# Optimization experiments

Hardware: AMD Instinct MI355X
Metric: run time of the kernel (lower is better)

## Reference

```python
import jax, jax.numpy as jnp
import numpy as np

B, T, E, H, D, V, L = 128, 100, 2048, 1024, 256, 2048, 2


def setup_inputs() -> dict:
    key = jax.random.key(0)
    ks = iter(jax.random.split(key, 32))
    def w(shape, s=0.02):
        return jax.random.normal(next(ks), shape, dtype=jnp.float32) * s
    return {
        "input_seq": jax.random.normal(next(ks), (B, T, E), dtype=jnp.float32),
        "h0": jax.random.normal(next(ks), (B, H), dtype=jnp.float32) * 0.1,
        "dt0": jax.random.normal(next(ks), (B, D), dtype=jnp.float32) * 0.1,
        "w2h_W0": w((E, 4 * H)), "w2h_b0": jnp.zeros((4 * H,), jnp.float32),
        "w2h_W1": w((E + H, 4 * H)), "w2h_b1": jnp.zeros((4 * H,), jnp.float32),
        "w2hr_W0": w((E, D)), "w2hr_b0": jnp.zeros((D,), jnp.float32),
        "w2hr_W1": w((E + H, D)), "w2hr_b1": jnp.zeros((D,), jnp.float32),
        "h2h_W0": w((H, 4 * H)), "h2h_b0": jnp.zeros((4 * H,), jnp.float32),
        "h2h_W1": w((H, 4 * H)), "h2h_b1": jnp.zeros((4 * H,), jnp.float32),
        "h2hr_W0": w((H, D)), "h2hr_b0": jnp.zeros((D,), jnp.float32),
        "h2hr_W1": w((H, D)), "h2hr_b1": jnp.zeros((D,), jnp.float32),
        "dc_W0": w((D, H)), "dc_W1": w((D, H)),
        "out_W": w((L * H, V)), "out_b": jnp.zeros((V,), jnp.float32),
    }


def reference(input_seq, h0, dt0,
              w2h_W0, w2h_b0, w2h_W1, w2h_b1,
              w2hr_W0, w2hr_b0, w2hr_W1, w2hr_b1,
              h2h_W0, h2h_b0, h2h_W1, h2h_b1,
              h2hr_W0, h2hr_b0, h2hr_W1, h2hr_b1,
              dc_W0, dc_W1, out_W, out_b):
    # SC-LSTM decoder (sclstm, n_layer=2, dropout=0, teacher forcing / gen=False)
    w2h = [(w2h_W0, w2h_b0), (w2h_W1, w2h_b1)]
    w2hr = [(w2hr_W0, w2hr_b0), (w2hr_W1, w2hr_b1)]
    h2h = [(h2h_W0, h2h_b0), (h2h_W1, h2h_b1)]
    h2hr = [(h2hr_W0, h2hr_b0), (h2hr_W1, h2hr_b1)]
    dc = [dc_W0, dc_W1]
    alpha = 1.0 / L

    # time-step inputs: SOS one-hot at t=0, then input_seq[:, t-1, :]
    sos = jnp.zeros((B, E), input_seq.dtype).at[:, 0].set(1.0)
    xs = jnp.concatenate([sos[:, None, :], input_seq[:, :-1, :]], axis=1)
    xs = jnp.swapaxes(xs, 0, 1)  # (T, B, E)

    h_init = jnp.stack([h0] * L)   # (L, B, H) -- both h and c init from last_hidden_t0
    c_init = jnp.stack([h0] * L)
    d_init = jnp.stack([dt0] * L)  # (L, B, D)

    def step(carry, x_t):
        h, c, d = carry
        # shared semantic-gate contribution: alpha * sum_i h2h_r[i](h_prev[i])
        r_common = alpha * sum(h[i] @ h2hr[i][0] + h2hr[i][1] for i in range(L))
        new_h, new_c, new_d = [], [], []
        for i in range(L):
            inp = x_t if i == 0 else jnp.concatenate([x_t] + new_h, axis=1)
            g = (inp @ w2h[i][0] + w2h[i][1]) + (h[i] @ h2h[i][0] + h2h[i][1])
            gi, gf, go, gc = jnp.split(g, 4, axis=1)
            gate_i = jax.nn.sigmoid(gi)
            gate_f = jax.nn.sigmoid(gf)
            gate_o = jax.nn.sigmoid(go)
            gate_r = jax.nn.sigmoid(inp @ w2hr[i][0] + w2hr[i][1] + r_common)
            dt = gate_r * d[i]
            cell = gate_f * c[i] + gate_i * jnp.tanh(gc) + jnp.tanh(dt @ dc[i])
            hid = gate_o * jnp.tanh(cell)
            new_h.append(hid); new_c.append(cell); new_d.append(dt)
        out_t = jnp.concatenate(new_h, axis=1) @ out_W + out_b  # (B, V)
        return (jnp.stack(new_h), jnp.stack(new_c), jnp.stack(new_d)), out_t

    _, outs = jax.lax.scan(step, (h_init, c_init, d_init), xs)
    return jnp.swapaxes(outs, 0, 1)  # (B, T, V)
```

## Files before the change

kernel.cpp:

```cpp
#include <hip/hip_runtime.h>

using u16 = unsigned short;
using u32 = unsigned int;
using f32x4 = __attribute__((ext_vector_type(4))) float;
using short8 = __attribute__((ext_vector_type(8))) short;

#define TT 100
#define BB 128
#define EE 2048
#define HH 1024
#define DD 256
#define VV 2048
#define H4 4096
#define NPRE 8704
#define MPRE (TT * BB)

__device__ __forceinline__ float bf2f(u16 u) { return __uint_as_float(((u32)u) << 16); }
__device__ __forceinline__ u16 f2bf(float f) {
  u32 x = __float_as_uint(f);
  x += 0x7fffu + ((x >> 16) & 1u);
  return (u16)(x >> 16);
}
__device__ __forceinline__ float sigm(float x) { return 1.0f / (1.0f + expf(-x)); }

__global__ __launch_bounds__(256) void build_xs(const float* __restrict__ inseq,
                                                u16* __restrict__ xs) {
  const int row = blockIdx.x;
  const int e0 = threadIdx.x << 3;
  const int t = row >> 7, b = row & 127;
  u16 v[8];
  if (t == 0) {
#pragma unroll
    for (int i = 0; i < 8; ++i) v[i] = 0;
    if (e0 == 0) v[0] = 0x3F80;
  } else {
    const float* src = inseq + ((size_t)b * TT + (t - 1)) * EE + e0;
#pragma unroll
    for (int i = 0; i < 8; ++i) v[i] = f2bf(src[i]);
  }
  uint4 o;
  o.x = (u32)v[0] | ((u32)v[1] << 16);
  o.y = (u32)v[2] | ((u32)v[3] << 16);
  o.z = (u32)v[4] | ((u32)v[5] << 16);
  o.w = (u32)v[6] | ((u32)v[7] << 16);
  *(uint4*)(xs + (size_t)row * EE + e0) = o;
}

__global__ __launch_bounds__(256) void tconv(const float* __restrict__ in, int ldin,
                                             u16* __restrict__ out, int ldout) {
  __shared__ float tile[32][33];
  const int k0 = blockIdx.y << 5, n0 = blockIdx.x << 5;
  const int tx = threadIdx.x, ty = threadIdx.y;
#pragma unroll
  for (int i = 0; i < 32; i += 8)
    tile[ty + i][tx] = in[(size_t)(k0 + ty + i) * ldin + n0 + tx];
  __syncthreads();
#pragma unroll
  for (int i = 0; i < 32; i += 8)
    out[(size_t)(n0 + ty + i) * ldout + k0 + tx] = f2bf(tile[tx][ty + i]);
}

__global__ __launch_bounds__(256) void k_biascat(
    const float* w2h_b0, const float* h2h_b0, const float* w2h_b1, const float* h2h_b1,
    const float* w2hr_b0, const float* w2hr_b1, float* biascat) {
  int g = blockIdx.x * 256 + threadIdx.x;
  if (g >= NPRE) return;
  float v;
  if (g < 4096) v = w2h_b0[g] + h2h_b0[g];
  else if (g < 8192) v = w2h_b1[g - 4096] + h2h_b1[g - 4096];
  else if (g < 8448) v = w2hr_b0[g - 8192];
  else v = w2hr_b1[g - 8448];
  biascat[g] = v;
}

__global__ __launch_bounds__(256) void k_init(const float* __restrict__ h0,
                                              const float* __restrict__ dt0,
                                              u16* __restrict__ hist, float* c0, float* c1,
                                              float* d0, float* d1) {
  int g = blockIdx.x * 256 + threadIdx.x;
  int b = g >> 11, j = g & 2047;
  float hv = h0[b * HH + (j & 1023)];
  hist[g] = f2bf(hv);
  if (j < HH) { c0[b * HH + j] = hv; c1[b * HH + j] = hv; }
  if (j < DD) { float dv = dt0[b * DD + j]; d0[b * DD + j] = dv; d1[b * DD + j] = dv; }
}

template <int MODE>
__global__ __launch_bounds__(256) void gemm_big(const u16* __restrict__ A,
                                                const u16* __restrict__ Bt,
                                                const float* __restrict__ bias,
                                                void* __restrict__ Cv, int N, int K) {
  __shared__ __align__(16) u16 lA[128 * 72];
  __shared__ __align__(16) u16 lB[128 * 72];
  const int tid = threadIdx.x;
  const int lane = tid & 63;
  const int wid = tid >> 6;
  const int wr = wid >> 1, wc = wid & 1;
  const int nt = N >> 7;
  const int bm = (blockIdx.x / nt) << 7;
  const int bn = (blockIdx.x % nt) << 7;
  f32x4 acc[4][4] = {};
  const int r = tid >> 1;
  const int kh = (tid & 1) << 5;
  const u16* ga = A + (size_t)(bm + r) * K + kh;
  const u16* gb = Bt + (size_t)(bn + r) * K + kh;
  for (int k0 = 0; k0 < K; k0 += 64) {
    uint4 a0 = *(const uint4*)(ga + k0);
    uint4 a1 = *(const uint4*)(ga + k0 + 8);
    uint4 a2 = *(const uint4*)(ga + k0 + 16);
    uint4 a3 = *(const uint4*)(ga + k0 + 24);
    uint4 b0 = *(const uint4*)(gb + k0);
    uint4 b1 = *(const uint4*)(gb + k0 + 8);
    uint4 b2 = *(const uint4*)(gb + k0 + 16);
    uint4 b3 = *(const uint4*)(gb + k0 + 24);
    __syncthreads();
    *(uint4*)(lA + r * 72 + kh) = a0;
    *(uint4*)(lA + r * 72 + kh + 8) = a1;
    *(uint4*)(lA + r * 72 + kh + 16) = a2;
    *(uint4*)(lA + r * 72 + kh + 24) = a3;
    *(uint4*)(lB + r * 72 + kh) = b0;
    *(uint4*)(lB + r * 72 + kh + 8) = b1;
    *(uint4*)(lB + r * 72 + kh + 16) = b2;
    *(uint4*)(lB + r * 72 + kh + 24) = b3;
    __syncthreads();
#pragma unroll
    for (int ks = 0; ks < 2; ++ks) {
      const int kk = ks * 32 + ((lane >> 4) << 3);
      short8 af[4], bf[4];
#pragma unroll
      for (int i = 0; i < 4; ++i) {
        af[i] = *(const short8*)(lA + (wr * 64 + i * 16 + (lane & 15)) * 72 + kk);
        bf[i] = *(const short8*)(lB + (wc * 64 + i * 16 + (lane & 15)) * 72 + kk);
      }
#pragma unroll
      for (int i = 0; i < 4; ++i)
#pragma unroll
        for (int j = 0; j < 4; ++j)
          acc[i][j] = __builtin_amdgcn_mfma_f32_16x16x32_bf16(af[i], bf[j], acc[i][j], 0, 0, 0);
    }
  }
#pragma unroll
  for (int i = 0; i < 4; ++i) {
#pragma unroll
    for (int j = 0; j < 4; ++j) {
      const int col = bn + wc * 64 + j * 16 + (lane & 15);
      const int rb = bm + wr * 64 + i * 16 + ((lane >> 4) << 2);
      const float bv = bias[col];
#pragma unroll
      for (int rg = 0; rg < 4; ++rg) {
        const int row = rb + rg;
        const float v = acc[i][j][rg] + bv;
        if (MODE == 0) {
          ((u16*)Cv)[(size_t)row * N + col] = f2bf(v);
        } else {
          const int tt = row >> 7, b = row & 127;
          ((float*)Cv)[((size_t)b * TT + tt) * VV + col] = v;
        }
      }
    }
  }
}

__device__ __forceinline__ void gemm64(const u16* __restrict__ A, int lda,
                                       const u16* __restrict__ Bt, int ldb, int K,
                                       u16* lA, u16* lB, f32x4 acc[2][2]) {
  const int tid = threadIdx.x;
  const int lane = tid & 63;
  const int wid = tid >> 6;
  const int wr = wid >> 1, wc = wid & 1;
  const int r = tid >> 2;
  const int kq = (tid & 3) << 4;
  const u16* ga = A + (size_t)r * lda + kq;
  const u16* gb = Bt + (size_t)r * ldb + kq;
  for (int k0 = 0; k0 < K; k0 += 64) {
    uint4 a0 = *(const uint4*)(ga + k0);
    uint4 a1 = *(const uint4*)(ga + k0 + 8);
    uint4 b0 = *(const uint4*)(gb + k0);
    uint4 b1 = *(const uint4*)(gb + k0 + 8);
    __syncthreads();
    *(uint4*)(lA + r * 72 + kq) = a0;
    *(uint4*)(lA + r * 72 + kq + 8) = a1;
    *(uint4*)(lB + r * 72 + kq) = b0;
    *(uint4*)(lB + r * 72 + kq + 8) = b1;
    __syncthreads();
#pragma unroll
    for (int ks = 0; ks < 2; ++ks) {
      const int kk = ks * 32 + ((lane >> 4) << 3);
      const short8 af0 = *(const short8*)(lA + (wr * 32 + (lane & 15)) * 72 + kk);
      const short8 af1 = *(const short8*)(lA + (wr * 32 + 16 + (lane & 15)) * 72 + kk);
      const short8 bf0 = *(const short8*)(lB + (wc * 32 + (lane & 15)) * 72 + kk);
      const short8 bf1 = *(const short8*)(lB + (wc * 32 + 16 + (lane & 15)) * 72 + kk);
      acc[0][0] = __builtin_amdgcn_mfma_f32_16x16x32_bf16(af0, bf0, acc[0][0], 0, 0, 0);
      acc[0][1] = __builtin_amdgcn_mfma_f32_16x16x32_bf16(af0, bf1, acc[0][1], 0, 0, 0);
      acc[1][0] = __builtin_amdgcn_mfma_f32_16x16x32_bf16(af1, bf0, acc[1][0], 0, 0, 0);
      acc[1][1] = __builtin_amdgcn_mfma_f32_16x16x32_bf16(af1, bf1, acc[1][1], 0, 0, 0);
    }
  }
  __syncthreads();
}

__device__ __forceinline__ void gemm_ccA(const u16* __restrict__ Bt, const u16* lA, u16* lB,
                                         f32x4 acc[2][2]) {
  const int tid = threadIdx.x;
  const int lane = tid & 63;
  const int wid = tid >> 6;
  const int wr = wid >> 1, wc = wid & 1;
  const int r = tid >> 2;
  const int kq = (tid & 3) << 4;
  const u16* gb = Bt + (size_t)r * DD + kq;
  for (int k0 = 0; k0 < 256; k0 += 64) {
    uint4 b0 = *(const uint4*)(gb + k0);
    uint4 b1 = *(const uint4*)(gb + k0 + 8);
    __syncthreads();
    *(uint4*)(lB + r * 72 + kq) = b0;
    *(uint4*)(lB + r * 72 + kq + 8) = b1;
    __syncthreads();
#pragma unroll
    for (int ks = 0; ks < 2; ++ks) {
      const int kk = ks * 32 + ((lane >> 4) << 3);
      const int ka = k0 + kk;
      const short8 af0 = *(const short8*)(lA + (wr * 32 + (lane & 15)) * 264 + ka);
      const short8 af1 = *(const short8*)(lA + (wr * 32 + 16 + (lane & 15)) * 264 + ka);
      const short8 bf0 = *(const short8*)(lB + (wc * 32 + (lane & 15)) * 72 + kk);
      const short8 bf1 = *(const short8*)(lB + (wc * 32 + 16 + (lane & 15)) * 72 + kk);
      acc[0][0] = __builtin_amdgcn_mfma_f32_16x16x32_bf16(af0, bf0, acc[0][0], 0, 0, 0);
      acc[0][1] = __builtin_amdgcn_mfma_f32_16x16x32_bf16(af0, bf1, acc[0][1], 0, 0, 0);
      acc[1][0] = __builtin_amdgcn_mfma_f32_16x16x32_bf16(af1, bf0, acc[1][0], 0, 0, 0);
      acc[1][1] = __builtin_amdgcn_mfma_f32_16x16x32_bf16(af1, bf1, acc[1][1], 0, 0, 0);
    }
  }
  __syncthreads();
}

#define EPI(...)                                                          \
  do {                                                                    \
    _Pragma("unroll") for (int ei = 0; ei < 2; ++ei) {                    \
      _Pragma("unroll") for (int ej = 0; ej < 2; ++ej) {                  \
        const int col = n0 + wc * 32 + ej * 16 + (lane & 15);             \
        const int rb = m0 + wr * 32 + ei * 16 + ((lane >> 4) << 2);       \
        _Pragma("unroll") for (int rg = 0; rg < 4; ++rg) {                \
          const int row = rb + rg;                                        \
          const float av = acc[ei][ej][rg];                               \
          __VA_ARGS__                                                     \
        }                                                                 \
      }                                                                   \
    }                                                                     \
  } while (0)

struct SeqArgs {
  const u16* Pcat;
  const u16* h2h0T;
  const u16* w1sT;
  const u16* hrsT;
  const u16* w2hr1hT;
  const u16* dc0T;
  const u16* dc1T;
  const float* hb0;
  const float* hb1;
  u16* hist;
  float* g0buf;
  float* g1p0;
  float* g1p1;
  float* rcp0;
  float* rcp1;
  float* c0;
  float* c1;
  float* d0;
  float* d1;
  u16* dt1bf;
};

__global__ __launch_bounds__(256) void stage1(SeqArgs a, int t) {
  __shared__ __align__(16) u16 ldsA[64 * 72];
  __shared__ __align__(16) u16 ldsB[64 * 72];
  const int tid = threadIdx.x, lane = tid & 63, wid = tid >> 6;
  const int wr = wid >> 1, wc = wid & 1;
  const int wg = blockIdx.x;
  const size_t slot0 = (size_t)t * (BB * 2048);
  const u16* px = a.Pcat + (size_t)t * (BB * NPRE);
  if (wg < 128) {
    const int m0 = (wg >> 6) << 6, n0 = (wg & 63) << 6;
    f32x4 acc[2][2] = {};
    gemm64(a.hist + slot0 + (size_t)m0 * 2048, 2048, a.h2h0T + (size_t)n0 * HH, HH, HH,
           ldsA, ldsB, acc);
    EPI(a.g0buf[row * H4 + col] = av + bf2f(px[(size_t)row * NPRE + col]););
  } else if (wg < 136) {
    const int jid = wg - 128;
    const int m0 = (jid >> 2) << 6, n0 = (jid & 3) << 6;
    f32x4 acc[2][2] = {};
    gemm64(a.hist + slot0 + (size_t)m0 * 2048, 2048, a.hrsT + (size_t)n0 * 2048, 2048, HH,
           ldsA, ldsB, acc);
    EPI(a.rcp0[row * DD + col] = av;);
  } else {
    const int jid = wg - 136;
    const int m0 = (jid >> 2) << 6, n0 = (jid & 3) << 6;
    f32x4 acc[2][2] = {};
    gemm64(a.hist + slot0 + (size_t)m0 * 2048 + 1024, 2048,
           a.hrsT + (size_t)n0 * 2048 + 1024, 2048, HH, ldsA, ldsB, acc);
    EPI(a.rcp1[row * DD + col] = av;);
  }
}

__global__ __launch_bounds__(256) void stage2(SeqArgs a, int t) {
  __shared__ __align__(16) u16 ldsA[64 * 264];
  __shared__ __align__(16) u16 ldsB[64 * 72];
  const int tid = threadIdx.x, lane = tid & 63, wid = tid >> 6;
  const int wr = wid >> 1, wc = wid & 1;
  const int wg = blockIdx.x;
  const size_t slot0 = (size_t)t * (BB * 2048);
  const size_t slot1 = slot0 + BB * 2048;
  const u16* px = a.Pcat + (size_t)t * (BB * NPRE);
  const int par = t & 1;
  if (wg < 32) {
    const int m0 = (wg >> 4) << 6, n0 = (wg & 15) << 6;
    {
      const int r = tid >> 2, kb = (tid & 3) << 6;
      const int b = m0 + r;
      const float* rp0 = a.rcp0 + b * DD;
      const float* rp1 = a.rcp1 + b * DD;
      const float* dold = a.d0 + par * (BB * DD) + b * DD;
      float* dnew = a.d0 + (par ^ 1) * (BB * DD) + b * DD;
      const u16* pxr = px + (size_t)b * NPRE + 8192;
      for (int kk = 0; kk < 64; ++kk) {
        const int k = kb + kk;
        const float rc = 0.5f * (rp0[k] + rp1[k] + a.hb0[k] + a.hb1[k]);
        const float dt = sigm(bf2f(pxr[k]) + rc) * dold[k];
        if (n0 == 0) dnew[k] = dt;
        ldsA[r * 264 + k] = f2bf(dt);
      }
    }
    f32x4 acc[2][2] = {};
    gemm_ccA(a.dc0T + (size_t)n0 * DD, ldsA, ldsB, acc);
    EPI(const float gi = a.g0buf[row * H4 + col];
        const float gf = a.g0buf[row * H4 + HH + col];
        const float go = a.g0buf[row * H4 + 2 * HH + col];
        const float gc = a.g0buf[row * H4 + 3 * HH + col];
        float c = sigm(gf) * a.c0[row * HH + col] + sigm(gi) * tanhf(gc) + tanhf(av);
        a.c0[row * HH + col] = c;
        a.hist[slot1 + (size_t)row * 2048 + col] = f2bf(sigm(go) * tanhf(c)););
  } else if (wg < 40) {
    const int jid = wg - 32;
    const int rr = (jid << 4) + (tid >> 4);
    const int cc = 1024 + ((tid & 15) << 6);
    const u16* srcp = a.hist + slot0 + (size_t)rr * 2048 + cc;
    u16* dstp = a.hist + slot1 + (size_t)rr * 2048 + cc;
#pragma unroll
    for (int q = 0; q < 8; ++q) *(uint4*)(dstp + q * 8) = *(const uint4*)(srcp + q * 8);
  }
}

__global__ __launch_bounds__(256) void stage3(SeqArgs a, int t) {
  __shared__ __align__(16) u16 ldsA[64 * 72];
  __shared__ __align__(16) u16 ldsB[64 * 72];
  const int tid = threadIdx.x, lane = tid & 63, wid = tid >> 6;
  const int wr = wid >> 1, wc = wid & 1;
  const int wg = blockIdx.x;
  const size_t slot1 = (size_t)(t + 1) * (BB * 2048);
  const u16* px = a.Pcat + (size_t)t * (BB * NPRE);
  const int par = t & 1;
  if (wg < 128) {
    const int m0 = (wg >> 6) << 6, n0 = (wg & 63) << 6;
    f32x4 acc[2][2] = {};
    gemm64(a.hist + slot1 + (size_t)m0 * 2048, 2048, a.w1sT + (size_t)n0 * 2048, 2048, HH,
           ldsA, ldsB, acc);
    EPI(a.g1p0[row * H4 + col] = av + bf2f(px[(size_t)row * NPRE + 4096 + col]););
  } else if (wg < 256) {
    const int jid = wg - 128;
    const int m0 = (jid >> 6) << 6, n0 = (jid & 63) << 6;
    f32x4 acc[2][2] = {};
    gemm64(a.hist + slot1 + (size_t)m0 * 2048 + 1024, 2048,
           a.w1sT + (size_t)n0 * 2048 + 1024, 2048, HH, ldsA, ldsB, acc);
    EPI(a.g1p1[row * H4 + col] = av;);
  } else {
    const int jid = wg - 256;
    const int m0 = (jid >> 2) << 6, n0 = (jid & 3) << 6;
    f32x4 acc[2][2] = {};
    gemm64(a.hist + slot1 + (size_t)m0 * 2048, 2048, a.w2hr1hT + (size_t)n0 * HH, HH, HH,
           ldsA, ldsB, acc);
    EPI(const float rc =
            0.5f * (a.rcp0[row * DD + col] + a.rcp1[row * DD + col] + a.hb0[col] + a.hb1[col]);
        const float r1 = bf2f(px[(size_t)row * NPRE + 8448 + col]) + rc + av;
        const float dt = sigm(r1) * a.d1[par * (BB * DD) + row * DD + col];
        a.d1[(par ^ 1) * (BB * DD) + row * DD + col] = dt;
        a.dt1bf[row * DD + col] = f2bf(dt););
  }
}

__global__ __launch_bounds__(256) void stage4(SeqArgs a, int t) {
  __shared__ __align__(16) u16 ldsA[64 * 72];
  __shared__ __align__(16) u16 ldsB[64 * 72];
  const int tid = threadIdx.x, lane = tid & 63, wid = tid >> 6;
  const int wr = wid >> 1, wc = wid & 1;
  const int wg = blockIdx.x;
  const size_t slot1 = (size_t)(t + 1) * (BB * 2048);
  const int m0 = (wg >> 4) << 6, n0 = (wg & 15) << 6;
  f32x4 acc[2][2] = {};
  gemm64(a.dt1bf + (size_t)m0 * DD, DD, a.dc1T + (size_t)n0 * DD, DD, DD, ldsA, ldsB, acc);
  EPI(const float gi = a.g1p0[row * H4 + col] + a.g1p1[row * H4 + col];
      const float gf = a.g1p0[row * H4 + HH + col] + a.g1p1[row * H4 + HH + col];
      const float go = a.g1p0[row * H4 + 2 * HH + col] + a.g1p1[row * H4 + 2 * HH + col];
      const float gc = a.g1p0[row * H4 + 3 * HH + col] + a.g1p1[row * H4 + 3 * HH + col];
      float c = sigm(gf) * a.c1[row * HH + col] + sigm(gi) * tanhf(gc) + tanhf(av);
      a.c1[row * HH + col] = c;
      a.hist[slot1 + (size_t)row * 2048 + 1024 + col] = f2bf(sigm(go) * tanhf(c)););
}

extern "C" void kernel_launch(void* const* d_in, const int* in_sizes, int n_in,
                              void* d_out, int out_size, void* d_ws, size_t ws_size,
                              hipStream_t stream) {
  const float* in_seq  = (const float*)d_in[0];
  const float* h0      = (const float*)d_in[1];
  const float* dt0     = (const float*)d_in[2];
  const float* w2h_W0  = (const float*)d_in[3];
  const float* w2h_b0  = (const float*)d_in[4];
  const float* w2h_W1  = (const float*)d_in[5];
  const float* w2h_b1  = (const float*)d_in[6];
  const float* w2hr_W0 = (const float*)d_in[7];
  const float* w2hr_b0 = (const float*)d_in[8];
  const float* w2hr_W1 = (const float*)d_in[9];
  const float* w2hr_b1 = (const float*)d_in[10];
  const float* h2h_W0  = (const float*)d_in[11];
  const float* h2h_b0  = (const float*)d_in[12];
  const float* h2h_W1  = (const float*)d_in[13];
  const float* h2h_b1  = (const float*)d_in[14];
  const float* h2hr_W0 = (const float*)d_in[15];
  const float* h2hr_b0 = (const float*)d_in[16];
  const float* h2hr_W1 = (const float*)d_in[17];
  const float* h2hr_b1 = (const float*)d_in[18];
  const float* dc_W0   = (const float*)d_in[19];
  const float* dc_W1   = (const float*)d_in[20];
  const float* out_W   = (const float*)d_in[21];
  const float* out_b   = (const float*)d_in[22];
  float* out = (float*)d_out;

  char* w = (char*)d_ws;
  auto alloc = [&](size_t bytes) {
    char* p = w;
    w += (bytes + 255) & ~(size_t)255;
    return p;
  };
  u16* xs      = (u16*)alloc((size_t)MPRE * EE * 2);
  u16* BpreT   = (u16*)alloc((size_t)NPRE * EE * 2);
  u16* Pcat    = (u16*)alloc((size_t)MPRE * NPRE * 2);
  u16* h2h0T   = (u16*)alloc((size_t)H4 * HH * 2);
  u16* w1sT    = (u16*)alloc((size_t)H4 * 2048 * 2);
  u16* hrsT    = (u16*)alloc((size_t)DD * 2048 * 2);
  u16* w2hr1hT = (u16*)alloc((size_t)DD * HH * 2);
  u16* dc0T    = (u16*)alloc((size_t)HH * DD * 2);
  u16* dc1T    = (u16*)alloc((size_t)HH * DD * 2);
  u16* outWT   = (u16*)alloc((size_t)VV * 2048 * 2);
  float* biascat = (float*)alloc((size_t)NPRE * 4);
  u16* hist    = (u16*)alloc((size_t)(TT + 1) * BB * 2048 * 2);
  float* g0buf = (float*)alloc((size_t)BB * H4 * 4);
  float* g1p0  = (float*)alloc((size_t)BB * H4 * 4);
  float* g1p1  = (float*)alloc((size_t)BB * H4 * 4);
  float* rcp0  = (float*)alloc((size_t)BB * DD * 4);
  float* rcp1  = (float*)alloc((size_t)BB * DD * 4);
  float* c0    = (float*)alloc((size_t)BB * HH * 4);
  float* c1    = (float*)alloc((size_t)BB * HH * 4);
  float* d0    = (float*)alloc((size_t)2 * BB * DD * 4);
  float* d1    = (float*)alloc((size_t)2 * BB * DD * 4);
  u16* dt1bf   = (u16*)alloc((size_t)BB * DD * 2);

  build_xs<<<MPRE, 256, 0, stream>>>(in_seq, xs);

  dim3 tb(32, 8);
  tconv<<<dim3(128, 64), tb, 0, stream>>>(w2h_W0, 4096, BpreT, 2048);
  tconv<<<dim3(128, 64), tb, 0, stream>>>(w2h_W1, 4096, BpreT + (size_t)4096 * 2048, 2048);
  tconv<<<dim3(8, 64), tb, 0, stream>>>(w2hr_W0, 256, BpreT + (size_t)8192 * 2048, 2048);
  tconv<<<dim3(8, 64), tb, 0, stream>>>(w2hr_W1, 256, BpreT + (size_t)8448 * 2048, 2048);
  tconv<<<dim3(128, 32), tb, 0, stream>>>(h2h_W0, 4096, h2h0T, 1024);
  tconv<<<dim3(128, 32), tb, 0, stream>>>(w2h_W1 + (size_t)2048 * 4096, 4096, w1sT, 2048);
  tconv<<<dim3(128, 32), tb, 0, stream>>>(h2h_W1, 4096, w1sT + 1024, 2048);
  tconv<<<dim3(8, 32), tb, 0, stream>>>(h2hr_W0, 256, hrsT, 2048);
  tconv<<<dim3(8, 32), tb, 0, stream>>>(h2hr_W1, 256, hrsT + 1024, 2048);
  tconv<<<dim3(8, 32), tb, 0, stream>>>(w2hr_W1 + (size_t)2048 * 256, 256, w2hr1hT, 1024);
  tconv<<<dim3(32, 8), tb, 0, stream>>>(dc_W0, 1024, dc0T, 256);
  tconv<<<dim3(32, 8), tb, 0, stream>>>(dc_W1, 1024, dc1T, 256);
  tconv<<<dim3(64, 64), tb, 0, stream>>>(out_W, 2048, outWT, 2048);

  k_biascat<<<(NPRE + 255) / 256, 256, 0, stream>>>(w2h_b0, h2h_b0, w2h_b1, h2h_b1,
                                                    w2hr_b0, w2hr_b1, biascat);
  k_init<<<(BB * 2048) / 256, 256, 0, stream>>>(h0, dt0, hist, c0, c1, d0, d1);

  gemm_big<0><<<(MPRE / 128) * (NPRE / 128), 256, 0, stream>>>(xs, BpreT, biascat, Pcat,
                                                               NPRE, EE);

  SeqArgs sa;
  sa.Pcat = Pcat; sa.h2h0T = h2h0T; sa.w1sT = w1sT; sa.hrsT = hrsT;
  sa.w2hr1hT = w2hr1hT; sa.dc0T = dc0T; sa.dc1T = dc1T;
  sa.hb0 = h2hr_b0; sa.hb1 = h2hr_b1;
  sa.hist = hist; sa.g0buf = g0buf; sa.g1p0 = g1p0; sa.g1p1 = g1p1;
  sa.rcp0 = rcp0; sa.rcp1 = rcp1; sa.c0 = c0; sa.c1 = c1;
  sa.d0 = d0; sa.d1 = d1; sa.dt1bf = dt1bf;

  for (int t = 0; t < TT; ++t) {
    stage1<<<144, 256, 0, stream>>>(sa, t);
    stage2<<<40, 256, 0, stream>>>(sa, t);
    stage3<<<264, 256, 0, stream>>>(sa, t);
    stage4<<<32, 256, 0, stream>>>(sa, t);
  }

  gemm_big<1><<<(MPRE / 128) * (VV / 128), 256, 0, stream>>>(hist + (size_t)BB * 2048, outWT,
                                                             out_b, out, VV, 2048);
}
```

Measured before the change: 13.00 ms.

## Split hidden history per layer, move layer-1 recurrent GEMM earlier, prefetch GEMM tiles

The interleaved hidden history is split into separate per-layer buffers, so the per-step copy of layer-1 hidden state is no longer needed. The layer-1 recurrent GEMM (h1_prev @ h2h_W1) moves from stage 3 into stage 1, where it depends only on the previous step and runs alongside the layer-0 GEMM; this shrinks the stage-3 grid. The inner gemm64 and gemm_ccA loops now prefetch four K-tiles into registers to hide global load latency. The cost is higher register pressure and a separate output GEMM kernel that reads from two A buffers.

New measurement: 17.71 ms. 1.36x slower.

```diff
diff --git a/kernel.cpp b/kernel.cpp
--- a/kernel.cpp
+++ b/kernel.cpp
@@ -75,21 +75,24 @@
 
 __global__ __launch_bounds__(256) void k_init(const float* __restrict__ h0,
                                               const float* __restrict__ dt0,
-                                              u16* __restrict__ hist, float* c0, float* c1,
+                                              u16* __restrict__ hist0,
+                                              u16* __restrict__ hist1,
+                                              float* c0, float* c1,
                                               float* d0, float* d1) {
   int g = blockIdx.x * 256 + threadIdx.x;
-  int b = g >> 11, j = g & 2047;
-  float hv = h0[b * HH + (j & 1023)];
-  hist[g] = f2bf(hv);
-  if (j < HH) { c0[b * HH + j] = hv; c1[b * HH + j] = hv; }
+  int b = g >> 10, j = g & 1023;
+  float hv = h0[b * HH + j];
+  u16 hb = f2bf(hv);
+  hist0[g] = hb;
+  hist1[g] = hb;
+  c0[g] = hv; c1[g] = hv;
   if (j < DD) { float dv = dt0[b * DD + j]; d0[b * DD + j] = dv; d1[b * DD + j] = dv; }
 }
 
-template <int MODE>
-__global__ __launch_bounds__(256) void gemm_big(const u16* __restrict__ A,
+__global__ __launch_bounds__(256) void gemm_pre(const u16* __restrict__ A,
                                                 const u16* __restrict__ Bt,
                                                 const float* __restrict__ bias,
-                                                void* __restrict__ Cv, int N, int K) {
+                                                u16* __restrict__ C, int N, int K) {
   __shared__ __align__(16) u16 lA[128 * 72];
   __shared__ __align__(16) u16 lB[128 * 72];
   const int tid = threadIdx.x;
@@ -149,13 +152,81 @@
 #pragma unroll
       for (int rg = 0; rg < 4; ++rg) {
         const int row = rb + rg;
-        const float v = acc[i][j][rg] + bv;
-        if (MODE == 0) {
-          ((u16*)Cv)[(size_t)row * N + col] = f2bf(v);
-        } else {
-          const int tt = row >> 7, b = row & 127;
-          ((float*)Cv)[((size_t)b * TT + tt) * VV + col] = v;
-        }
+        C[(size_t)row * N + col] = f2bf(acc[i][j][rg] + bv);
+      }
+    }
+  }
+}
+
+__global__ __launch_bounds__(256) void gemm_out(const u16* __restrict__ A0,
+                                                const u16* __restrict__ A1,
+                                                const u16* __restrict__ Bt,
+                                                const float* __restrict__ bias,
+                                                float* __restrict__ out) {
+  __shared__ __align__(16) u16 lA[128 * 72];
+  __shared__ __align__(16) u16 lB[128 * 72];
+  const int tid = threadIdx.x;
+  const int lane = tid & 63;
+  const int wid = tid >> 6;
+  const int wr = wid >> 1, wc = wid & 1;
+  const int nt = VV >> 7;
+  const int bm = (blockIdx.x / nt) << 7;
+  const int bn = (blockIdx.x % nt) << 7;
+  f32x4 acc[4][4] = {};
+  const int r = tid >> 1;
+  const int kh = (tid & 1) << 5;
+  const u16* ga0 = A0 + (size_t)(bm + r) * 1024;
+  const u16* ga1 = A1 + (size_t)(bm + r) * 1024;
+  const u16* gb = Bt + (size_t)(bn + r) * 2048 + kh;
+  for (int k0 = 0; k0 < 2048; k0 += 64) {
+    const int col = k0 + kh;
+    const u16* gp = (col < 1024) ? (ga0 + col) : (ga1 + (col - 1024));
+    uint4 a0 = *(const uint4*)(gp);
+    uint4 a1 = *(const uint4*)(gp + 8);
+    uint4 a2 = *(const uint4*)(gp + 16);
+    uint4 a3 = *(const uint4*)(gp + 24);
+    uint4 b0 = *(const uint4*)(gb + k0);
+    uint4 b1 = *(const uint4*)(gb + k0 + 8);
+    uint4 b2 = *(const uint4*)(gb + k0 + 16);
+    uint4 b3 = *(const uint4*)(gb + k0 + 24);
+    __syncthreads();
+    *(uint4*)(lA + r * 72 + kh) = a0;
+    *(uint4*)(lA + r * 72 + kh + 8) = a1;
+    *(uint4*)(lA + r * 72 + kh + 16) = a2;
+    *(uint4*)(lA + r * 72 + kh + 24) = a3;
+    *(uint4*)(lB + r * 72 + kh) = b0;
+    *(uint4*)(lB + r * 72 + kh + 8) = b1;
+    *(uint4*)(lB + r * 72 + kh + 16) = b2;
+    *(uint4*)(lB + r * 72 + kh + 24) = b3;
+    __syncthreads();
+#pragma unroll
+    for (int ks = 0; ks < 2; ++ks) {
+      const int kk = ks * 32 + ((lane >> 4) << 3);
+      short8 af[4], bf[4];
+#pragma unroll
+      for (int i = 0; i < 4; ++i) {
+        af[i] = *(const short8*)(lA + (wr * 64 + i * 16 + (lane & 15)) * 72 + kk);
+        bf[i] = *(const short8*)(lB + (wc * 64 + i * 16 + (lane & 15)) * 72 + kk);
+      }
+#pragma unroll
+      for (int i = 0; i < 4; ++i)
+#pragma unroll
+        for (int j = 0; j < 4; ++j)
+          acc[i][j] = __builtin_amdgcn_mfma_f32_16x16x32_bf16(af[i], bf[j], acc[i][j], 0, 0, 0);
+    }
+  }
+#pragma unroll
+  for (int i = 0; i < 4; ++i) {
+#pragma unroll
+    for (int j = 0; j < 4; ++j) {
+      const int col = bn + wc * 64 + j * 16 + (lane & 15);
+      const int rb = bm + wr * 64 + i * 16 + ((lane >> 4) << 2);
+      const float bv = bias[col];
+#pragma unroll
+      for (int rg = 0; rg < 4; ++rg) {
+        const int row = rb + rg;
+        const int tt = row >> 7, b = row & 127;
+        out[((size_t)b * TT + tt) * VV + col] = acc[i][j][rg] + bv;
       }
     }
   }
@@ -172,28 +243,44 @@
   const int kq = (tid & 3) << 4;
   const u16* ga = A + (size_t)r * lda + kq;
   const u16* gb = Bt + (size_t)r * ldb + kq;
-  for (int k0 = 0; k0 < K; k0 += 64) {
-    uint4 a0 = *(const uint4*)(ga + k0);
-    uint4 a1 = *(const uint4*)(ga + k0 + 8);
-    uint4 b0 = *(const uint4*)(gb + k0);
-    uint4 b1 = *(const uint4*)(gb + k0 + 8);
-    __syncthreads();
-    *(uint4*)(lA + r * 72 + kq) = a0;
-    *(uint4*)(lA + r * 72 + kq + 8) = a1;
-    *(uint4*)(lB + r * 72 + kq) = b0;
-    *(uint4*)(lB + r * 72 + kq + 8) = b1;
-    __syncthreads();
-#pragma unroll
-    for (int ks = 0; ks < 2; ++ks) {
-      const int kk = ks * 32 + ((lane >> 4) << 3);
-      const short8 af0 = *(const short8*)(lA + (wr * 32 + (lane & 15)) * 72 + kk);
-      const short8 af1 = *(const short8*)(lA + (wr * 32 + 16 + (lane & 15)) * 72 + kk);
-      const short8 bf0 = *(const short8*)(lB + (wc * 32 + (lane & 15)) * 72 + kk);
-      const short8 bf1 = *(const short8*)(lB + (wc * 32 + 16 + (lane & 15)) * 72 + kk);
-      acc[0][0] = __builtin_amdgcn_mfma_f32_16x16x32_bf16(af0, bf0, acc[0][0], 0, 0, 0);
-      acc[0][1] = __builtin_amdgcn_mfma_f32_16x16x32_bf16(af0, bf1, acc[0][1], 0, 0, 0);
-      acc[1][0] = __builtin_amdgcn_mfma_f32_16x16x32_bf16(af1, bf0, acc[1][0], 0, 0, 0);
-      acc[1][1] = __builtin_amdgcn_mfma_f32_16x16x32_bf16(af1, bf1, acc[1][1], 0, 0, 0);
+  const int nk = K >> 6;
+  uint4 pa0[4], pa1[4], pb0[4], pb1[4];
+#pragma unroll
+  for (int s = 0; s < 4; ++s) {
+    pa0[s] = *(const uint4*)(ga + s * 64);
+    pa1[s] = *(const uint4*)(ga + s * 64 + 8);
+    pb0[s] = *(const uint4*)(gb + s * 64);
+    pb1[s] = *(const uint4*)(gb + s * 64 + 8);
+  }
+#pragma unroll 1
+  for (int base = 0; base < nk; base += 4) {
+#pragma unroll
+    for (int s = 0; s < 4; ++s) {
+      const int i = base + s;
+      __syncthreads();
+      *(uint4*)(lA + r * 72 + kq) = pa0[s];
+      *(uint4*)(lA + r * 72 + kq + 8) = pa1[s];
+      *(uint4*)(lB + r * 72 + kq) = pb0[s];
+      *(uint4*)(lB + r * 72 + kq + 8) = pb1[s];
+      __syncthreads();
+      if (i + 4 < nk) {
+        pa0[s] = *(const uint4*)(ga + (size_t)(i + 4) * 64);
+        pa1[s] = *(const uint4*)(ga + (size_t)(i + 4) * 64 + 8);
+        pb0[s] = *(const uint4*)(gb + (size_t)(i + 4) * 64);
+        pb1[s] = *(const uint4*)(gb + (size_t)(i + 4) * 64 + 8);
+      }
+#pragma unroll
+      for (int ks = 0; ks < 2; ++ks) {
+        const int kk = ks * 32 + ((lane >> 4) << 3);
+        const short8 af0 = *(const short8*)(lA + (wr * 32 + (lane & 15)) * 72 + kk);
+        const short8 af1 = *(const short8*)(lA + (wr * 32 + 16 + (lane & 15)) * 72 + kk);
+        const short8 bf0 = *(const short8*)(lB + (wc * 32 + (lane & 15)) * 72 + kk);
+        const short8 bf1 = *(const short8*)(lB + (wc * 32 + 16 + (lane & 15)) * 72 + kk);
+        acc[0][0] = __builtin_amdgcn_mfma_f32_16x16x32_bf16(af0, bf0, acc[0][0], 0, 0, 0);
+        acc[0][1] = __builtin_amdgcn_mfma_f32_16x16x32_bf16(af0, bf1, acc[0][1], 0, 0, 0);
+        acc[1][0] = __builtin_amdgcn_mfma_f32_16x16x32_bf16(af1, bf0, acc[1][0], 0, 0, 0);
+        acc[1][1] = __builtin_amdgcn_mfma_f32_16x16x32_bf16(af1, bf1, acc[1][1], 0, 0, 0);
+      }
     }
   }
   __syncthreads();
@@ -208,12 +295,18 @@
   const int r = tid >> 2;
   const int kq = (tid & 3) << 4;
   const u16* gb = Bt + (size_t)r * DD + kq;
-  for (int k0 = 0; k0 < 256; k0 += 64) {
-    uint4 b0 = *(const uint4*)(gb + k0);
-    uint4 b1 = *(const uint4*)(gb + k0 + 8);
+  uint4 pb0[4], pb1[4];
+#pragma unroll
+  for (int s = 0; s < 4; ++s) {
+    pb0[s] = *(const uint4*)(gb + s * 64);
+    pb1[s] = *(const uint4*)(gb + s * 64 + 8);
+  }
+#pragma unroll
+  for (int s = 0; s < 4; ++s) {
+    const int k0 = s * 64;
     __syncthreads();
-    *(uint4*)(lB + r * 72 + kq) = b0;
-    *(uint4*)(lB + r * 72 + kq + 8) = b1;
+    *(uint4*)(lB + r * 72 + kq) = pb0[s];
+    *(uint4*)(lB + r * 72 + kq + 8) = pb1[s];
     __syncthreads();
 #pragma unroll
     for (int ks = 0; ks < 2; ++ks) {
@@ -257,7 +350,8 @@
   const u16* dc1T;
   const float* hb0;
   const float* hb1;
-  u16* hist;
+  u16* hist0;
+  u16* hist1;
   float* g0buf;
   float* g1p0;
   float* g1p1;
@@ -270,112 +364,102 @@
   u16* dt1bf;
 };
 
-__global__ __launch_bounds__(256) void stage1(SeqArgs a, int t) {
+__global__ __launch_bounds__(256) void sk1(SeqArgs a, int t) {
   __shared__ __align__(16) u16 ldsA[64 * 72];
   __shared__ __align__(16) u16 ldsB[64 * 72];
   const int tid = threadIdx.x, lane = tid & 63, wid = tid >> 6;
   const int wr = wid >> 1, wc = wid & 1;
   const int wg = blockIdx.x;
-  const size_t slot0 = (size_t)t * (BB * 2048);
+  const u16* h0t = a.hist0 + (size_t)t * (BB * 1024);
+  const u16* h1t = a.hist1 + (size_t)t * (BB * 1024);
   const u16* px = a.Pcat + (size_t)t * (BB * NPRE);
   if (wg < 128) {
     const int m0 = (wg >> 6) << 6, n0 = (wg & 63) << 6;
     f32x4 acc[2][2] = {};
-    gemm64(a.hist + slot0 + (size_t)m0 * 2048, 2048, a.h2h0T + (size_t)n0 * HH, HH, HH,
+    gemm64(h0t + (size_t)m0 * 1024, 1024, a.h2h0T + (size_t)n0 * HH, HH, HH,
            ldsA, ldsB, acc);
     EPI(a.g0buf[row * H4 + col] = av + bf2f(px[(size_t)row * NPRE + col]););
   } else if (wg < 136) {
     const int jid = wg - 128;
     const int m0 = (jid >> 2) << 6, n0 = (jid & 3) << 6;
     f32x4 acc[2][2] = {};
-    gemm64(a.hist + slot0 + (size_t)m0 * 2048, 2048, a.hrsT + (size_t)n0 * 2048, 2048, HH,
+    gemm64(h0t + (size_t)m0 * 1024, 1024, a.hrsT + (size_t)n0 * 2048, 2048, HH,
            ldsA, ldsB, acc);
     EPI(a.rcp0[row * DD + col] = av;);
-  } else {
+  } else if (wg < 144) {
     const int jid = wg - 136;
     const int m0 = (jid >> 2) << 6, n0 = (jid & 3) << 6;
     f32x4 acc[2][2] = {};
-    gemm64(a.hist + slot0 + (size_t)m0 * 2048 + 1024, 2048,
-           a.hrsT + (size_t)n0 * 2048 + 1024, 2048, HH, ldsA, ldsB, acc);
+    gemm64(h1t + (size_t)m0 * 1024, 1024, a.hrsT + (size_t)n0 * 2048 + 1024, 2048, HH,
+           ldsA, ldsB, acc);
     EPI(a.rcp1[row * DD + col] = av;);
-  }
-}
-
-__global__ __launch_bounds__(256) void stage2(SeqArgs a, int t) {
+  } else {
+    const int jid = wg - 144;
+    const int m0 = (jid >> 6) << 6, n0 = (jid & 63) << 6;
+    f32x4 acc[2][2] = {};
+    gemm64(h1t + (size_t)m0 * 1024, 1024, a.w1sT + (size_t)n0 * 2048 + 1024, 2048, HH,
+           ldsA, ldsB, acc);
+    EPI(a.g1p1[row * H4 + col] = av;);
+  }
+}
+
+__global__ __launch_bounds__(256) void sk2(SeqArgs a, int t) {
   __shared__ __align__(16) u16 ldsA[64 * 264];
   __shared__ __align__(16) u16 ldsB[64 * 72];
   const int tid = threadIdx.x, lane = tid & 63, wid = tid >> 6;
   const int wr = wid >> 1, wc = wid & 1;
   const int wg = blockIdx.x;
-  const size_t slot0 = (size_t)t * (BB * 2048);
-  const size_t slot1 = slot0 + BB * 2048;
   const u16* px = a.Pcat + (size_t)t * (BB * NPRE);
+  u16* h0n = a.hist0 + (size_t)(t + 1) * (BB * 1024);
   const int par = t & 1;
-  if (wg < 32) {
-    const int m0 = (wg >> 4) << 6, n0 = (wg & 15) << 6;
-    {
-      const int r = tid >> 2, kb = (tid & 3) << 6;
-      const int b = m0 + r;
-      const float* rp0 = a.rcp0 + b * DD;
-      const float* rp1 = a.rcp1 + b * DD;
-      const float* dold = a.d0 + par * (BB * DD) + b * DD;
-      float* dnew = a.d0 + (par ^ 1) * (BB * DD) + b * DD;
-      const u16* pxr = px + (size_t)b * NPRE + 8192;
-      for (int kk = 0; kk < 64; ++kk) {
-        const int k = kb + kk;
-        const float rc = 0.5f * (rp0[k] + rp1[k] + a.hb0[k] + a.hb1[k]);
-        const float dt = sigm(bf2f(pxr[k]) + rc) * dold[k];
-        if (n0 == 0) dnew[k] = dt;
-        ldsA[r * 264 + k] = f2bf(dt);
-      }
-    }
-    f32x4 acc[2][2] = {};
-    gemm_ccA(a.dc0T + (size_t)n0 * DD, ldsA, ldsB, acc);
-    EPI(const float gi = a.g0buf[row * H4 + col];
-        const float gf = a.g0buf[row * H4 + HH + col];
-        const float go = a.g0buf[row * H4 + 2 * HH + col];
-        const float gc = a.g0buf[row * H4 + 3 * HH + col];
-        float c = sigm(gf) * a.c0[row * HH + col] + sigm(gi) * tanhf(gc) + tanhf(av);
-        a.c0[row * HH + col] = c;
-        a.hist[slot1 + (size_t)row * 2048 + col] = f2bf(sigm(go) * tanhf(c)););
-  } else if (wg < 40) {
-    const int jid = wg - 32;
-    const int rr = (jid << 4) + (tid >> 4);
-    const int cc = 1024 + ((tid & 15) << 6);
-    const u16* srcp = a.hist + slot0 + (size_t)rr * 2048 + cc;
-    u16* dstp = a.hist + slot1 + (size_t)rr * 2048 + cc;
-#pragma unroll
-    for (int q = 0; q < 8; ++q) *(uint4*)(dstp + q * 8) = *(const uint4*)(srcp + q * 8);
-  }
-}
-
-__global__ __launch_bounds__(256) void stage3(SeqArgs a, int t) {
+  const int m0 = (wg >> 4) << 6, n0 = (wg & 15) << 6;
+  {
+    const int r = tid >> 2, kb = (tid & 3) << 6;
+    const int b = m0 + r;
+    const float* rp0 = a.rcp0 + b * DD;
+    const float* rp1 = a.rcp1 + b * DD;
+    const float* dold = a.d0 + par * (BB * DD) + b * DD;
+    float* dnew = a.d0 + (par ^ 1) * (BB * DD) + b * DD;
+    const u16* pxr = px + (size_t)b * NPRE + 8192;
+    for (int kk = 0; kk < 64; ++kk) {
+      const int k = kb + kk;
+      const float rc = 0.5f * (rp0[k] + rp1[k] + a.hb0[k] + a.hb1[k]);
+      const float dt = sigm(bf2f(pxr[k]) + rc) * dold[k];
+      if (n0 == 0) dnew[k] = dt;
+      ldsA[r * 264 + k] = f2bf(dt);
+    }
+  }
+  f32x4 acc[2][2] = {};
+  gemm_ccA(a.dc0T + (size_t)n0 * DD, ldsA, ldsB, acc);
+  EPI(const float gi = a.g0buf[row * H4 + col];
+      const float gf = a.g0buf[row * H4 + HH + col];
+      const float go = a.g0buf[row * H4 + 2 * HH + col];
+      const float gc = a.g0buf[row * H4 + 3 * HH + col];
+      float c = sigm(gf) * a.c0[row * HH + col] + sigm(gi) * tanhf(gc) + tanhf(av);
+      a.c0[row * HH + col] = c;
+      h0n[(size_t)row * 1024 + col] = f2bf(sigm(go) * tanhf(c)););
+}
+
+__global__ __launch_bounds__(256) void sk3(SeqArgs a, int t) {
   __shared__ __align__(16) u16 ldsA[64 * 72];
   __shared__ __align__(16) u16 ldsB[64 * 72];
   const int tid = threadIdx.x, lane = tid & 63, wid = tid >> 6;
   const int wr = wid >> 1, wc = wid & 1;
   const int wg = blockIdx.x;
-  const size_t slot1 = (size_t)(t + 1) * (BB * 2048);
+  const u16* h0n = a.hist0 + (size_t)(t + 1) * (BB * 1024);
   const u16* px = a.Pcat + (size_t)t * (BB * NPRE);
   const int par = t & 1;
   if (wg < 128) {
     const int m0 = (wg >> 6) << 6, n0 = (wg & 63) << 6;
     f32x4 acc[2][2] = {};
-    gemm64(a.hist + slot1 + (size_t)m0 * 2048, 2048, a.w1sT + (size_t)n0 * 2048, 2048, HH,
+    gemm64(h0n + (size_t)m0 * 1024, 1024, a.w1sT + (size_t)n0 * 2048, 2048, HH,
            ldsA, ldsB, acc);
     EPI(a.g1p0[row * H4 + col] = av + bf2f(px[(size_t)row * NPRE + 4096 + col]););
-  } else if (wg < 256) {
+  } else {
     const int jid = wg - 128;
-    const int m0 = (jid >> 6) << 6, n0 = (jid & 63) << 6;
-    f32x4 acc[2][2] = {};
-    gemm64(a.hist + slot1 + (size_t)m0 * 2048 + 1024, 2048,
-           a.w1sT + (size_t)n0 * 2048 + 1024, 2048, HH, ldsA, ldsB, acc);
-    EPI(a.g1p1[row * H4 + col] = av;);
-  } else {
-    const int jid = wg - 256;
     const int m0 = (jid >> 2) << 6, n0 = (jid & 3) << 6;
     f32x4 acc[2][2] = {};
-    gemm64(a.hist + slot1 + (size_t)m0 * 2048, 2048, a.w2hr1hT + (size_t)n0 * HH, HH, HH,
+    gemm64(h0n + (size_t)m0 * 1024, 1024, a.w2hr1hT + (size_t)n0 * HH, HH, HH,
            ldsA, ldsB, acc);
     EPI(const float rc =
             0.5f * (a.rcp0[row * DD + col] + a.rcp1[row * DD + col] + a.hb0[col] + a.hb1[col]);
@@ -386,13 +470,13 @@
   }
 }
 
-__global__ __launch_bounds__(256) void stage4(SeqArgs a, int t) {
+__global__ __launch_bounds__(256) void sk4(SeqArgs a, int t) {
   __shared__ __align__(16) u16 ldsA[64 * 72];
   __shared__ __align__(16) u16 ldsB[64 * 72];
   const int tid = threadIdx.x, lane = tid & 63, wid = tid >> 6;
   const int wr = wid >> 1, wc = wid & 1;
   const int wg = blockIdx.x;
-  const size_t slot1 = (size_t)(t + 1) * (BB * 2048);
+  u16* h1n = a.hist1 + (size_t)(t + 1) * (BB * 1024);
   const int m0 = (wg >> 4) << 6, n0 = (wg & 15) << 6;
   f32x4 acc[2][2] = {};
   gemm64(a.dt1bf + (size_t)m0 * DD, DD, a.dc1T + (size_t)n0 * DD, DD, DD, ldsA, ldsB, acc);
@@ -402,7 +486,7 @@
       const float gc = a.g1p0[row * H4 + 3 * HH + col] + a.g1p1[row * H4 + 3 * HH + col];
       float c = sigm(gf) * a.c1[row * HH + col] + sigm(gi) * tanhf(gc) + tanhf(av);
       a.c1[row * HH + col] = c;
-      a.hist[slot1 + (size_t)row * 2048 + 1024 + col] = f2bf(sigm(go) * tanhf(c)););
+      h1n[(size_t)row * 1024 + col] = f2bf(sigm(go) * tanhf(c)););
 }
 
 extern "C" void kernel_launch(void* const* d_in, const int* in_sizes, int n_in,
@@ -450,7 +534,8 @@
   u16* dc1T    = (u16*)alloc((size_t)HH * DD * 2);
   u16* outWT   = (u16*)alloc((size_t)VV * 2048 * 2);
   float* biascat = (float*)alloc((size_t)NPRE * 4);
-  u16* hist    = (u16*)alloc((size_t)(TT + 1) * BB * 2048 * 2);
+  u16* hist0   = (u16*)alloc((size_t)(TT + 1) * BB * 1024 * 2);
+  u16* hist1   = (u16*)alloc((size_t)(TT + 1) * BB * 1024 * 2);
   float* g0buf = (float*)alloc((size_t)BB * H4 * 4);
   float* g1p0  = (float*)alloc((size_t)BB * H4 * 4);
   float* g1p1  = (float*)alloc((size_t)BB * H4 * 4);
@@ -481,26 +566,27 @@
 
   k_biascat<<<(NPRE + 255) / 256, 256, 0, stream>>>(w2h_b0, h2h_b0, w2h_b1, h2h_b1,
                                                     w2hr_b0, w2hr_b1, biascat);
-  k_init<<<(BB * 2048) / 256, 256, 0, stream>>>(h0, dt0, hist, c0, c1, d0, d1);
-
-  gemm_big<0><<<(MPRE / 128) * (NPRE / 128), 256, 0, stream>>>(xs, BpreT, biascat, Pcat,
-                                                               NPRE, EE);
+  k_init<<<(BB * 1024) / 256, 256, 0, stream>>>(h0, dt0, hist0, hist1, c0, c1, d0, d1);
+
+  gemm_pre<<<(MPRE / 128) * (NPRE / 128), 256, 0, stream>>>(xs, BpreT, biascat, Pcat,
+                                                            NPRE, EE);
 
   SeqArgs sa;
   sa.Pcat = Pcat; sa.h2h0T = h2h0T; sa.w1sT = w1sT; sa.hrsT = hrsT;
   sa.w2hr1hT = w2hr1hT; sa.dc0T = dc0T; sa.dc1T = dc1T;
   sa.hb0 = h2hr_b0; sa.hb1 = h2hr_b1;
-  sa.hist = hist; sa.g0buf = g0buf; sa.g1p0 = g1p0; sa.g1p1 = g1p1;
+  sa.hist0 = hist0; sa.hist1 = hist1;
+  sa.g0buf = g0buf; sa.g1p0 = g1p0; sa.g1p1 = g1p1;
   sa.rcp0 = rcp0; sa.rcp1 = rcp1; sa.c0 = c0; sa.c1 = c1;
   sa.d0 = d0; sa.d1 = d1; sa.dt1bf = dt1bf;
 
   for (int t = 0; t < TT; ++t) {
-    stage1<<<144, 256, 0, stream>>>(sa, t);
-    stage2<<<40, 256, 0, stream>>>(sa, t);
-    stage3<<<264, 256, 0, stream>>>(sa, t);
-    stage4<<<32, 256, 0, stream>>>(sa, t);
-  }
-
-  gemm_big<1><<<(MPRE / 128) * (VV / 128), 256, 0, stream>>>(hist + (size_t)BB * 2048, outWT,
-                                                             out_b, out, VV, 2048);
-}
+    sk1<<<272, 256, 0, stream>>>(sa, t);
+    sk2<<<32, 256, 0, stream>>>(sa, t);
+    sk3<<<136, 256, 0, stream>>>(sa, t);
+    sk4<<<32, 256, 0, stream>>>(sa, t);
+  }
+
+  gemm_out<<<(MPRE / 128) * (VV / 128), 256, 0, stream>>>(
+      hist0 + (size_t)BB * 1024, hist1 + (size_t)BB * 1024, outWT, out_b, out);
+}
```
